# Optimization experiments

Measured on AMD Instinct MI355X. Metric: run time of the kernel, lower is better.

The kernel has to match this reference:

```python
import jax, jax.numpy as jnp
from jax import lax
import numpy as np

NPOINT, RADIUS, NSAMPLE = 1024, 0.2, 32
MLP = [64, 64, 128]
IN_CH = 35  # 3 coord channels + 32 point features
EPS = 1e-5


def farthest_point_sample(xyz, npoint):
    # xyz: (B, N, 3) -> (B, npoint) int32. Deterministic start at index 0.
    B, N, _ = xyz.shape

    def step(carry, _):
        dist, farthest = carry  # (B,N), (B,)
        centroid = jnp.take_along_axis(xyz, farthest[:, None, None], axis=1)  # (B,1,3)
        d = jnp.sum((xyz - centroid) ** 2, axis=-1)  # (B,N)
        dist = jnp.minimum(dist, d)
        nxt = jnp.argmax(dist, axis=-1).astype(jnp.int32)
        return (dist, nxt), farthest

    init = (jnp.full((B, N), 1e10, xyz.dtype), jnp.zeros((B,), jnp.int32))
    _, idxs = lax.scan(step, init, None, length=npoint)
    return idxs.T  # (B, npoint)


def gather_points(points, idx):
    # points: (B, N, C); idx: (B, ...) int -> (B, ..., C)
    return jax.vmap(lambda p, i: p[i])(points, idx)


def query_ball_point(radius, nsample, xyz, new_xyz):
    # xyz: (B,N,3), new_xyz: (B,S,3) -> (B,S,nsample) int32
    B, N, _ = xyz.shape
    sqrdists = jnp.sum((new_xyz[:, :, None, :] - xyz[:, None, :, :]) ** 2, axis=-1)  # (B,S,N)
    group_idx = jnp.where(sqrdists > radius ** 2, N, jnp.arange(N, dtype=jnp.int32))
    group_idx = jnp.sort(group_idx, axis=-1)[:, :, :nsample]
    first = group_idx[:, :, :1]
    return jnp.where(group_idx == N, first, group_idx)


def sa_forward(xyz, points, params):
    B, N, C = xyz.shape
    fps_idx = farthest_point_sample(xyz, NPOINT)
    new_xyz = gather_points(xyz, fps_idx)  # (B,S,3)
    idx = query_ball_point(RADIUS, NSAMPLE, xyz, new_xyz)  # (B,S,K)
    grouped_xyz = gather_points(xyz, idx)  # (B,S,K,3)
    grouped_xyz_norm = grouped_xyz - new_xyz[:, :, None, :]
    grouped_points = gather_points(points, idx)  # (B,S,K,D)
    new_points = jnp.concatenate([grouped_xyz_norm, grouped_points], axis=-1)  # (B,S,K,Cin)
    x = new_points.transpose(0, 3, 2, 1)  # (B, Cin, K, S)
    for w, b, g, be in params:
        x = jnp.einsum('oi,biks->boks', w, x) + b[None, :, None, None]  # 1x1 conv
        mean = x.mean(axis=(0, 2, 3), keepdims=True)  # BatchNorm2d, training mode
        var = x.var(axis=(0, 2, 3), keepdims=True)
        x = (x - mean) / jnp.sqrt(var + EPS)
        x = jax.nn.relu(g[None, :, None, None] * x + be[None, :, None, None])
    new_points_out = x.max(axis=2)  # max over nsample -> (B, Cout, S)
    return new_xyz, new_points_out


def setup_inputs() -> dict:
    key = jax.random.key(0)
    ks = jax.random.split(key, 16)
    B, N, D = 16, 4096, 32
    inp = {
        'xyz': jax.random.uniform(ks[0], (B, N, 3), dtype=jnp.float32),
        'points': jax.random.normal(ks[1], (B, N, D), dtype=jnp.float32),
    }
    last = IN_CH
    for li, out_ch in enumerate(MLP):
        inp[f'w{li}'] = jax.random.normal(ks[2 + 4 * li], (out_ch, last), dtype=jnp.float32) * 0.05
        inp[f'b{li}'] = jnp.zeros((out_ch,), jnp.float32)
        inp[f'g{li}'] = jnp.ones((out_ch,), jnp.float32)
        inp[f'be{li}'] = jnp.zeros((out_ch,), jnp.float32)
        last = out_ch
    return inp


def reference(xyz, points, w0, b0, g0, be0, w1, b1, g1, be1, w2, b2, g2, be2):
    params = [(w0, b0, g0, be0), (w1, b1, g1, be1), (w2, b2, g2, be2)]
    return sa_forward(xyz, points, params)
```

## Files before the change

### kernel.cpp

```cpp
#include <hip/hip_runtime.h>
#include <hip/hip_bf16.h>
#include <stdint.h>

#pragma clang fp contract(off)

#define BATCH   16
#define NPTS    4096
#define NPOINT  1024
#define NSAMPLE 32
#define NPOS    (BATCH*NPOINT*NSAMPLE)
#define NBLK    (NPOS/128)
#define NGRP    (BATCH*NPOINT)
#define EPSV    1e-5f

typedef unsigned short ushort_t;
typedef unsigned int uint_t;
typedef unsigned long long u64;
typedef __attribute__((ext_vector_type(8))) short bf16x8;
typedef __attribute__((ext_vector_type(4))) float f32x4;
typedef __attribute__((ext_vector_type(2))) float f32x2;

__device__ inline ushort_t f2bf(float f) {
    uint_t u = __float_as_uint(f);
    u += 0x7fffu + ((u >> 16) & 1u);
    return (ushort_t)(u >> 16);
}
__device__ inline uint_t pkbf(float a, float b) {
    __hip_bfloat162 h = __float22bfloat162_rn(make_float2(a, b));
    uint_t r; __builtin_memcpy(&r, &h, 4); return r;
}
__device__ inline bf16x8 asbf(uint4 u) {
    bf16x8 v; __builtin_memcpy(&v, &u, 16); return v;
}
__device__ inline void unpack8(uint4 u, float* f) {
    f[0] = __uint_as_float(u.x << 16); f[1] = __uint_as_float(u.x & 0xffff0000u);
    f[2] = __uint_as_float(u.y << 16); f[3] = __uint_as_float(u.y & 0xffff0000u);
    f[4] = __uint_as_float(u.z << 16); f[5] = __uint_as_float(u.z & 0xffff0000u);
    f[6] = __uint_as_float(u.w << 16); f[7] = __uint_as_float(u.w & 0xffff0000u);
}

__global__ __launch_bounds__(256) void prep_w(const float* __restrict__ w0,
                                              const float* __restrict__ w1,
                                              const float* __restrict__ w2,
                                              ushort_t* __restrict__ Wp0,
                                              ushort_t* __restrict__ Wx0,
                                              ushort_t* __restrict__ Wp1,
                                              ushort_t* __restrict__ Wp2) {
    const int t = blockIdx.x * 256 + threadIdx.x;
    const int stride = gridDim.x * 256;
    for (int i = t; i < 64 * 32; i += stride) { int ch = i >> 5, k = i & 31; Wp0[i] = f2bf(w0[ch * 35 + 3 + k]); }
    for (int i = t; i < 64 * 4;  i += stride) { int ch = i >> 2, q = i & 3;  Wx0[i] = (q < 3) ? f2bf(w0[ch * 35 + q]) : (ushort_t)0; }
    for (int i = t; i < 64 * 64; i += stride) Wp1[i] = f2bf(w1[i]);
    for (int i = t; i < 128 * 64; i += stride) Wp2[i] = f2bf(w2[i]);
}

#define DPP_MAX_STAGE(CTRL) do {                                              \
    uint_t _lo2 = __builtin_amdgcn_update_dpp(lo, lo, CTRL, 0xf, 0xf, false); \
    uint_t _hi2 = __builtin_amdgcn_update_dpp(hi, hi, CTRL, 0xf, 0xf, false); \
    u64 _o = ((u64)_hi2 << 32) | _lo2;                                        \
    u64 _v = ((u64)hi << 32) | lo;                                            \
    bool _g = _o > _v;                                                        \
    lo = _g ? _lo2 : lo; hi = _g ? _hi2 : hi;                                 \
} while (0)

__global__ __launch_bounds__(256) void fps_kernel(const float* __restrict__ xyz,
                                                  float* __restrict__ new_xyz) {
    __shared__ float4 lxyz[NPTS];
    __shared__ u64 wbest[2][4];
    __shared__ int fpsidx[NPOINT];
    const int b = blockIdx.x;
    const int tid = threadIdx.x;
    const float* base = xyz + (size_t)b * NPTS * 3;
    for (int n = tid; n < NPTS; n += 256) {
        lxyz[n] = make_float4(base[3 * n], base[3 * n + 1], base[3 * n + 2], 0.f);
    }
    __syncthreads();

    f32x2 px[8], py[8], pz[8], dist[8];
    uint_t lowc[16];
#pragma unroll
    for (int j = 0; j < 8; j++) {
        float4 v0 = lxyz[tid + (2 * j) * 256];
        float4 v1 = lxyz[tid + (2 * j + 1) * 256];
        px[j] = (f32x2){v0.x, v1.x};
        py[j] = (f32x2){v0.y, v1.y};
        pz[j] = (f32x2){v0.z, v1.z};
        dist[j] = (f32x2){1e10f, 1e10f};
        lowc[2 * j] = ~(uint_t)(tid + (2 * j) * 256);
        lowc[2 * j + 1] = ~(uint_t)(tid + (2 * j + 1) * 256);
    }
    if (tid == 0) fpsidx[0] = 0;
    int cur = 0;
    const int lane = tid & 63, wid = tid >> 6;

    for (int it = 1; it < NPOINT; ++it) {
        float4 c = lxyz[cur];
        const f32x2 cx = (f32x2){c.x, c.x};
        const f32x2 cy = (f32x2){c.y, c.y};
        const f32x2 cz = (f32x2){c.z, c.z};
        u64 t[8];
#pragma unroll
        for (int j = 0; j < 8; j++) {
            f32x2 dx = px[j] - cx;
            f32x2 dy = py[j] - cy;
            f32x2 dz = pz[j] - cz;
            f32x2 d = (dx * dx + dy * dy) + dz * dz;
            f32x2 nd = __builtin_elementwise_min(dist[j], d);
            dist[j] = nd;
            u64 e0 = ((u64)__float_as_uint(nd.x) << 32) | lowc[2 * j];
            u64 e1 = ((u64)__float_as_uint(nd.y) << 32) | lowc[2 * j + 1];
            t[j] = e0 > e1 ? e0 : e1;
        }
#pragma unroll
        for (int j = 0; j < 4; j++) { u64 o = t[j + 4]; t[j] = t[j] > o ? t[j] : o; }
        t[0] = t[0] > t[1] ? t[0] : t[1];
        t[2] = t[2] > t[3] ? t[2] : t[3];
        u64 v = t[0] > t[2] ? t[0] : t[2];

        uint_t lo = (uint_t)v, hi = (uint_t)(v >> 32);
        DPP_MAX_STAGE(0x111);
        DPP_MAX_STAGE(0x112);
        DPP_MAX_STAGE(0x114);
        DPP_MAX_STAGE(0x118);
        DPP_MAX_STAGE(0x142);
        DPP_MAX_STAGE(0x143);
        uint_t mlo = __builtin_amdgcn_readlane(lo, 63);
        uint_t mhi = __builtin_amdgcn_readlane(hi, 63);

        const int par = it & 1;
        if (lane == 0) wbest[par][wid] = ((u64)mhi << 32) | mlo;
        __syncthreads();
        u64 b0 = wbest[par][0], b1 = wbest[par][1];
        u64 b2 = wbest[par][2], b3 = wbest[par][3];
        u64 m01 = b0 > b1 ? b0 : b1;
        u64 m23 = b2 > b3 ? b2 : b3;
        u64 bb = m01 > m23 ? m01 : m23;
        cur = (int)(~(uint_t)bb) & (NPTS - 1);
        if (tid == 0) fpsidx[it] = cur;
    }
    __syncthreads();
    float* ob = new_xyz + (size_t)b * NPOINT * 3;
    for (int s = tid; s < NPOINT; s += 256) {
        float4 v = lxyz[fpsidx[s]];
        ob[3 * s + 0] = v.x; ob[3 * s + 1] = v.y; ob[3 * s + 2] = v.z;
    }
}

__global__ __launch_bounds__(256) void ballq_kernel(const float* __restrict__ xyz,
                                                    const float* __restrict__ new_xyz,
                                                    int* __restrict__ gidx) {
    const int gw = (int)((blockIdx.x * 256 + threadIdx.x) >> 6);
    const int lane = threadIdx.x & 63;
    const int b = gw / NPOINT, s = gw % NPOINT;
    const float* nb = new_xyz + ((size_t)b * NPOINT + s) * 3;
    const float cx = nb[0], cy = nb[1], cz = nb[2];
    const float* xb = xyz + (size_t)b * NPTS * 3;
    const float r2 = (float)(0.2 * 0.2);
    int cnt = 0;
    int first = -1;
    int* out = gidx + (size_t)gw * NSAMPLE;
    for (int j0 = 0; j0 < NPTS; j0 += 64) {
        int j = j0 + lane;
        float dx = __fsub_rn(xb[j * 3 + 0], cx);
        float dy = __fsub_rn(xb[j * 3 + 1], cy);
        float dz = __fsub_rn(xb[j * 3 + 2], cz);
        float d = __fadd_rn(__fadd_rn(__fmul_rn(dx, dx), __fmul_rn(dy, dy)),
                            __fmul_rn(dz, dz));
        bool pred = !(d > r2);
        u64 mask = __ballot(pred);
        if (first < 0 && mask != 0ull) first = j0 + (__ffsll((long long)mask) - 1);
        int before = __popcll(mask & ((1ull << lane) - 1ull));
        int slot = cnt + before;
        if (pred && slot < NSAMPLE) out[slot] = j;
        cnt += (int)__popcll(mask);
        if (cnt >= NSAMPLE) break;
    }
    if (cnt < NSAMPLE) {
        if (lane >= cnt && lane < NSAMPLE) out[lane] = first;
    }
}

__global__ __launch_bounds__(256) void conv1_mfma(const float* __restrict__ xyz,
                                                  const float* __restrict__ points,
                                                  const float* __restrict__ new_xyz,
                                                  const int* __restrict__ gidx,
                                                  const ushort_t* __restrict__ Wp0,
                                                  const ushort_t* __restrict__ Wx0,
                                                  const float* __restrict__ bias,
                                                  ushort_t* __restrict__ Y,
                                                  float* __restrict__ part_s,
                                                  float* __restrict__ part_q) {
    const int lane = threadIdx.x & 63, wid = threadIdx.x >> 6;
    const int l15 = lane & 15, quad = lane >> 4;
    const int p0 = blockIdx.x * 128 + wid * 32;

    bf16x8 Bp[4], Bx[4];
#pragma unroll
    for (int nt = 0; nt < 4; nt++) {
        const int ch = nt * 16 + l15;
        Bp[nt] = *(const bf16x8*)(Wp0 + (size_t)ch * 32 + quad * 8);
        uint4 bx = {0u, 0u, 0u, 0u};
        if (quad == 0) {
            uint2 wv = *(const uint2*)(Wx0 + ch * 4);
            bx.x = wv.x; bx.y = wv.y;
        }
        Bx[nt] = asbf(bx);
    }
    f32x4 acc[2][4];
#pragma unroll
    for (int mt = 0; mt < 2; mt++)
#pragma unroll
        for (int nt = 0; nt < 4; nt++) acc[mt][nt] = (f32x4){0.f, 0.f, 0.f, 0.f};

#pragma unroll
    for (int mt = 0; mt < 2; mt++) {
        const int p = p0 + mt * 16 + l15;
        const int b = p >> 15, s = (p & 32767) >> 5;
        const int j = gidx[p];
        const float* pr = points + ((size_t)(b * NPTS + j)) * 32 + quad * 8;
        float4 pa = *(const float4*)pr;
        float4 pb4 = *(const float4*)(pr + 4);
        uint4 ap;
        ap.x = pkbf(pa.x, pa.y);  ap.y = pkbf(pa.z, pa.w);
        ap.z = pkbf(pb4.x, pb4.y); ap.w = pkbf(pb4.z, pb4.w);
        bf16x8 Ap = asbf(ap);
        uint4 ax = {0u, 0u, 0u, 0u};
        if (quad == 0) {
            const float* xp = xyz + ((size_t)(b * NPTS + j)) * 3;
            const float* nz = new_xyz + ((size_t)(b * NPOINT + s)) * 3;
            float d0 = xp[0] - nz[0], d1 = xp[1] - nz[1], d2 = xp[2] - nz[2];
            ax.x = pkbf(d0, d1);
            ax.y = pkbf(d2, 0.f);
        }
        bf16x8 Ax = asbf(ax);
#pragma unroll
        for (int nt = 0; nt < 4; nt++) {
            acc[mt][nt] = __builtin_amdgcn_mfma_f32_16x16x32_bf16(Ap, Bp[nt], acc[mt][nt], 0, 0, 0);
            acc[mt][nt] = __builtin_amdgcn_mfma_f32_16x16x32_bf16(Ax, Bx[nt], acc[mt][nt], 0, 0, 0);
        }
    }
    float s_[4], q_[4];
#pragma unroll
    for (int nt = 0; nt < 4; nt++) { s_[nt] = 0.f; q_[nt] = 0.f; }
#pragma unroll
    for (int nt = 0; nt < 4; nt++) {
        const int ch = nt * 16 + l15;
        const float bs = bias[ch];
#pragma unroll
        for (int mt = 0; mt < 2; mt++) {
            const int pb = p0 + mt * 16 + quad * 4;
            float x0 = acc[mt][nt][0] + bs, x1 = acc[mt][nt][1] + bs;
            float x2 = acc[mt][nt][2] + bs, x3 = acc[mt][nt][3] + bs;
            uint_t p01 = pkbf(x0, x1), p23 = pkbf(x2, x3);
            Y[(size_t)(pb + 0) * 64 + ch] = (ushort_t)(p01 & 0xffffu);
            Y[(size_t)(pb + 1) * 64 + ch] = (ushort_t)(p01 >> 16);
            Y[(size_t)(pb + 2) * 64 + ch] = (ushort_t)(p23 & 0xffffu);
            Y[(size_t)(pb + 3) * 64 + ch] = (ushort_t)(p23 >> 16);
            float v0 = __uint_as_float(p01 << 16), v1 = __uint_as_float(p01 & 0xffff0000u);
            float v2 = __uint_as_float(p23 << 16), v3 = __uint_as_float(p23 & 0xffff0000u);
            s_[nt] += (v0 + v1) + (v2 + v3);
            q_[nt] += (v0 * v0 + v1 * v1) + (v2 * v2 + v3 * v3);
        }
    }
#pragma unroll
    for (int nt = 0; nt < 4; nt++) {
        s_[nt] += __shfl_xor(s_[nt], 16, 64); s_[nt] += __shfl_xor(s_[nt], 32, 64);
        q_[nt] += __shfl_xor(q_[nt], 16, 64); q_[nt] += __shfl_xor(q_[nt], 32, 64);
    }
    __shared__ float reds[4][4][16], redq[4][4][16];
    if (lane < 16) {
#pragma unroll
        for (int nt = 0; nt < 4; nt++) { reds[wid][nt][lane] = s_[nt]; redq[wid][nt][lane] = q_[nt]; }
    }
    __syncthreads();
    if (threadIdx.x < 16) {
#pragma unroll
        for (int nt = 0; nt < 4; nt++) {
            float ss = 0.f, qq = 0.f;
#pragma unroll
            for (int w = 0; w < 4; w++) { ss += reds[w][nt][threadIdx.x]; qq += redq[w][nt][threadIdx.x]; }
            const int ch = nt * 16 + threadIdx.x;
            part_s[(size_t)ch * NBLK + blockIdx.x] = ss;
            part_q[(size_t)ch * NBLK + blockIdx.x] = qq;
        }
    }
}

__global__ __launch_bounds__(256) void conv2_mfma(const ushort_t* __restrict__ Yin,
                                                  const float* __restrict__ scale,
                                                  const float* __restrict__ shift,
                                                  const ushort_t* __restrict__ Wp,
                                                  const float* __restrict__ bias,
                                                  ushort_t* __restrict__ Yout,
                                                  float* __restrict__ part_s,
                                                  float* __restrict__ part_q) {
    constexpr int IN = 64, OUT = 64, NT = 4;
    const int lane = threadIdx.x & 63, wid = threadIdx.x >> 6;
    const int l15 = lane & 15, quad = lane >> 4;
    const int p0 = blockIdx.x * 128 + wid * 32;

    float sc[2][8], sh[2][8];
#pragma unroll
    for (int kq = 0; kq < 2; kq++) {
        const int i0 = kq * 32 + quad * 8;
#pragma unroll
        for (int q = 0; q < 8; q++) { sc[kq][q] = scale[i0 + q]; sh[kq][q] = shift[i0 + q]; }
    }
    bf16x8 Bf[NT][2];
#pragma unroll
    for (int nt = 0; nt < NT; nt++)
#pragma unroll
        for (int kq = 0; kq < 2; kq++)
            Bf[nt][kq] = *(const bf16x8*)(Wp + (size_t)(nt * 16 + l15) * IN + kq * 32 + quad * 8);

    bf16x8 Af[2][2];
#pragma unroll
    for (int mt = 0; mt < 2; mt++)
#pragma unroll
        for (int kq = 0; kq < 2; kq++) {
            const ushort_t* yr = Yin + (size_t)(p0 + mt * 16 + l15) * IN + kq * 32 + quad * 8;
            uint4 u = *(const uint4*)yr;
            float f[8]; unpack8(u, f);
            float g0 = fmaxf(fmaf(f[0], sc[kq][0], sh[kq][0]), 0.f);
            float g1 = fmaxf(fmaf(f[1], sc[kq][1], sh[kq][1]), 0.f);
            float g2 = fmaxf(fmaf(f[2], sc[kq][2], sh[kq][2]), 0.f);
            float g3 = fmaxf(fmaf(f[3], sc[kq][3], sh[kq][3]), 0.f);
            float g4 = fmaxf(fmaf(f[4], sc[kq][4], sh[kq][4]), 0.f);
            float g5 = fmaxf(fmaf(f[5], sc[kq][5], sh[kq][5]), 0.f);
            float g6 = fmaxf(fmaf(f[6], sc[kq][6], sh[kq][6]), 0.f);
            float g7 = fmaxf(fmaf(f[7], sc[kq][7], sh[kq][7]), 0.f);
            uint4 a;
            a.x = pkbf(g0, g1); a.y = pkbf(g2, g3);
            a.z = pkbf(g4, g5); a.w = pkbf(g6, g7);
            Af[mt][kq] = asbf(a);
        }

    f32x4 acc[2][NT];
#pragma unroll
    for (int mt = 0; mt < 2; mt++)
#pragma unroll
        for (int nt = 0; nt < NT; nt++) acc[mt][nt] = (f32x4){0.f, 0.f, 0.f, 0.f};
#pragma unroll
    for (int mt = 0; mt < 2; mt++)
#pragma unroll
        for (int nt = 0; nt < NT; nt++) {
            acc[mt][nt] = __builtin_amdgcn_mfma_f32_16x16x32_bf16(Af[mt][0], Bf[nt][0], acc[mt][nt], 0, 0, 0);
            acc[mt][nt] = __builtin_amdgcn_mfma_f32_16x16x32_bf16(Af[mt][1], Bf[nt][1], acc[mt][nt], 0, 0, 0);
        }
    float s_[NT], q_[NT];
#pragma unroll
    for (int nt = 0; nt < NT; nt++) { s_[nt] = 0.f; q_[nt] = 0.f; }
#pragma unroll
    for (int nt = 0; nt < NT; nt++) {
        const int ch = nt * 16 + l15;
        const float bs = bias[ch];
#pragma unroll
        for (int mt = 0; mt < 2; mt++) {
            const int pb = p0 + mt * 16 + quad * 4;
            float x0 = acc[mt][nt][0] + bs, x1 = acc[mt][nt][1] + bs;
            float x2 = acc[mt][nt][2] + bs, x3 = acc[mt][nt][3] + bs;
            uint_t p01 = pkbf(x0, x1), p23 = pkbf(x2, x3);
            Yout[(size_t)(pb + 0) * OUT + ch] = (ushort_t)(p01 & 0xffffu);
            Yout[(size_t)(pb + 1) * OUT + ch] = (ushort_t)(p01 >> 16);
            Yout[(size_t)(pb + 2) * OUT + ch] = (ushort_t)(p23 & 0xffffu);
            Yout[(size_t)(pb + 3) * OUT + ch] = (ushort_t)(p23 >> 16);
            float v0 = __uint_as_float(p01 << 16), v1 = __uint_as_float(p01 & 0xffff0000u);
            float v2 = __uint_as_float(p23 << 16), v3 = __uint_as_float(p23 & 0xffff0000u);
            s_[nt] += (v0 + v1) + (v2 + v3);
            q_[nt] += (v0 * v0 + v1 * v1) + (v2 * v2 + v3 * v3);
        }
    }
#pragma unroll
    for (int nt = 0; nt < NT; nt++) {
        s_[nt] += __shfl_xor(s_[nt], 16, 64); s_[nt] += __shfl_xor(s_[nt], 32, 64);
        q_[nt] += __shfl_xor(q_[nt], 16, 64); q_[nt] += __shfl_xor(q_[nt], 32, 64);
    }
    __shared__ float reds[4][NT][16], redq[4][NT][16];
    if (lane < 16) {
#pragma unroll
        for (int nt = 0; nt < NT; nt++) { reds[wid][nt][lane] = s_[nt]; redq[wid][nt][lane] = q_[nt]; }
    }
    __syncthreads();
    if (threadIdx.x < 16) {
#pragma unroll
        for (int nt = 0; nt < NT; nt++) {
            float ss = 0.f, qq = 0.f;
#pragma unroll
            for (int w = 0; w < 4; w++) { ss += reds[w][nt][threadIdx.x]; qq += redq[w][nt][threadIdx.x]; }
            const int ch = nt * 16 + threadIdx.x;
            part_s[(size_t)ch * NBLK + blockIdx.x] = ss;
            part_q[(size_t)ch * NBLK + blockIdx.x] = qq;
        }
    }
}

__global__ __launch_bounds__(256) void conv3_mfma(const ushort_t* __restrict__ Yin,
                                                  const float* __restrict__ scale,
                                                  const float* __restrict__ shift,
                                                  const ushort_t* __restrict__ Wp,
                                                  const float* __restrict__ bias,
                                                  float* __restrict__ xmax,
                                                  float* __restrict__ xmin,
                                                  float* __restrict__ part_s,
                                                  float* __restrict__ part_q) {
    constexpr int IN = 64, NT = 8;
    const int lane = threadIdx.x & 63, wid = threadIdx.x >> 6;
    const int l15 = lane & 15, quad = lane >> 4;
    const int p0 = blockIdx.x * 128 + wid * 32;
    const int g = p0 >> 5;

    float sc[2][8], sh[2][8];
#pragma unroll
    for (int kq = 0; kq < 2; kq++) {
        const int i0 = kq * 32 + quad * 8;
#pragma unroll
        for (int q = 0; q < 8; q++) { sc[kq][q] = scale[i0 + q]; sh[kq][q] = shift[i0 + q]; }
    }
    bf16x8 Bf[NT][2];
#pragma unroll
    for (int nt = 0; nt < NT; nt++)
#pragma unroll
        for (int kq = 0; kq < 2; kq++)
            Bf[nt][kq] = *(const bf16x8*)(Wp + (size_t)(nt * 16 + l15) * IN + kq * 32 + quad * 8);

    bf16x8 Af[2][2];
#pragma unroll
    for (int mt = 0; mt < 2; mt++)
#pragma unroll
        for (int kq = 0; kq < 2; kq++) {
            const ushort_t* yr = Yin + (size_t)(p0 + mt * 16 + l15) * IN + kq * 32 + quad * 8;
            uint4 u = *(const uint4*)yr;
            float f[8]; unpack8(u, f);
            float g0 = fmaxf(fmaf(f[0], sc[kq][0], sh[kq][0]), 0.f);
            float g1 = fmaxf(fmaf(f[1], sc[kq][1], sh[kq][1]), 0.f);
            float g2 = fmaxf(fmaf(f[2], sc[kq][2], sh[kq][2]), 0.f);
            float g3 = fmaxf(fmaf(f[3], sc[kq][3], sh[kq][3]), 0.f);
            float g4 = fmaxf(fmaf(f[4], sc[kq][4], sh[kq][4]), 0.f);
            float g5 = fmaxf(fmaf(f[5], sc[kq][5], sh[kq][5]), 0.f);
            float g6 = fmaxf(fmaf(f[6], sc[kq][6], sh[kq][6]), 0.f);
            float g7 = fmaxf(fmaf(f[7], sc[kq][7], sh[kq][7]), 0.f);
            uint4 a;
            a.x = pkbf(g0, g1); a.y = pkbf(g2, g3);
            a.z = pkbf(g4, g5); a.w = pkbf(g6, g7);
            Af[mt][kq] = asbf(a);
        }

    f32x4 acc[2][NT];
#pragma unroll
    for (int mt = 0; mt < 2; mt++)
#pragma unroll
        for (int nt = 0; nt < NT; nt++) acc[mt][nt] = (f32x4){0.f, 0.f, 0.f, 0.f};
#pragma unroll
    for (int mt = 0; mt < 2; mt++)
#pragma unroll
        for (int nt = 0; nt < NT; nt++) {
            acc[mt][nt] = __builtin_amdgcn_mfma_f32_16x16x32_bf16(Af[mt][0], Bf[nt][0], acc[mt][nt], 0, 0, 0);
            acc[mt][nt] = __builtin_amdgcn_mfma_f32_16x16x32_bf16(Af[mt][1], Bf[nt][1], acc[mt][nt], 0, 0, 0);
        }
    float s_[NT], q_[NT], xm[NT], xn[NT];
#pragma unroll
    for (int nt = 0; nt < NT; nt++) { s_[nt] = 0.f; q_[nt] = 0.f; xm[nt] = -3e38f; xn[nt] = 3e38f; }
#pragma unroll
    for (int nt = 0; nt < NT; nt++) {
        const float bs = bias[nt * 16 + l15];
#pragma unroll
        for (int mt = 0; mt < 2; mt++) {
#pragma unroll
            for (int r = 0; r < 4; r++) {
                float x = acc[mt][nt][r] + bs;
                s_[nt] += x; q_[nt] += x * x;
                xm[nt] = fmaxf(xm[nt], x); xn[nt] = fminf(xn[nt], x);
            }
        }
    }
#pragma unroll
    for (int nt = 0; nt < NT; nt++) {
        s_[nt] += __shfl_xor(s_[nt], 16, 64); s_[nt] += __shfl_xor(s_[nt], 32, 64);
        q_[nt] += __shfl_xor(q_[nt], 16, 64); q_[nt] += __shfl_xor(q_[nt], 32, 64);
        xm[nt] = fmaxf(xm[nt], __shfl_xor(xm[nt], 16, 64));
        xm[nt] = fmaxf(xm[nt], __shfl_xor(xm[nt], 32, 64));
        xn[nt] = fminf(xn[nt], __shfl_xor(xn[nt], 16, 64));
        xn[nt] = fminf(xn[nt], __shfl_xor(xn[nt], 32, 64));
    }
    if (quad == 0) {
#pragma unroll
        for (int nt = 0; nt < NT; nt++) {
            const int ch = nt * 16 + l15;
            xmax[(size_t)g * 128 + ch] = xm[nt];
            xmin[(size_t)g * 128 + ch] = xn[nt];
        }
    }
    __shared__ float reds[4][NT][16], redq[4][NT][16];
    if (lane < 16) {
#pragma unroll
        for (int nt = 0; nt < NT; nt++) { reds[wid][nt][lane] = s_[nt]; redq[wid][nt][lane] = q_[nt]; }
    }
    __syncthreads();
    if (threadIdx.x < 16) {
#pragma unroll
        for (int nt = 0; nt < NT; nt++) {
            float ss = 0.f, qq = 0.f;
#pragma unroll
            for (int w = 0; w < 4; w++) { ss += reds[w][nt][threadIdx.x]; qq += redq[w][nt][threadIdx.x]; }
            const int ch = nt * 16 + threadIdx.x;
            part_s[(size_t)ch * NBLK + blockIdx.x] = ss;
            part_q[(size_t)ch * NBLK + blockIdx.x] = qq;
        }
    }
}

__global__ __launch_bounds__(256) void reduce_finalize(const float* __restrict__ part_s,
                                                       const float* __restrict__ part_q,
                                                       const float* __restrict__ g,
                                                       const float* __restrict__ be,
                                                       float* __restrict__ scale,
                                                       float* __restrict__ shift) {
    const int ch = blockIdx.x;
    const float* p1 = part_s + (size_t)ch * NBLK;
    const float* p2 = part_q + (size_t)ch * NBLK;
    float s = 0.f, q = 0.f;
    for (int i = threadIdx.x; i < NBLK; i += 256) { s += p1[i]; q += p2[i]; }
#pragma unroll
    for (int m = 1; m < 64; m <<= 1) { s += __shfl_xor(s, m, 64); q += __shfl_xor(q, m, 64); }
    __shared__ float ls[4], lq[4];
    const int lane = threadIdx.x & 63, wid = threadIdx.x >> 6;
    if (lane == 0) { ls[wid] = s; lq[wid] = q; }
    __syncthreads();
    if (threadIdx.x == 0) {
        float ssum = ls[0] + ls[1] + ls[2] + ls[3];
        float qsum = lq[0] + lq[1] + lq[2] + lq[3];
        float mean = ssum * (1.f / (float)NPOS);
        float var = qsum * (1.f / (float)NPOS) - mean * mean;
        float inv = 1.f / sqrtf(var + EPSV);
        float sc = g[ch] * inv;
        scale[ch] = sc;
        shift[ch] = be[ch] - mean * sc;
    }
}

__global__ __launch_bounds__(256) void final2_kernel(const float* __restrict__ xmax,
                                                     const float* __restrict__ xmin,
                                                     const float* __restrict__ scale,
                                                     const float* __restrict__ shift,
                                                     float* __restrict__ out) {
    __shared__ float buf[128][129];
    const int b = blockIdx.x >> 3;
    const int s0 = (blockIdx.x & 7) * 128;
    const int tid = threadIdx.x;
    for (int i = tid; i < 128 * 128; i += 256) {
        const int si = i >> 7, ch = i & 127;
        const size_t g = (size_t)(b * NPOINT + s0 + si);
        const float sc = scale[ch], sh = shift[ch];
        const float xM = xmax[g * 128 + ch];
        const float xN = xmin[g * 128 + ch];
        const float X = sc > 0.f ? xM : xN;
        buf[si][ch] = fmaxf(fmaf(X, sc, sh), 0.f);
    }
    __syncthreads();
    for (int i = tid; i < 128 * 128; i += 256) {
        const int ch = i >> 7, si = i & 127;
        out[((size_t)(b * 128 + ch)) * NPOINT + s0 + si] = buf[si][ch];
    }
}

extern "C" void kernel_launch(void* const* d_in, const int* in_sizes, int n_in,
                              void* d_out, int out_size, void* d_ws, size_t ws_size,
                              hipStream_t stream) {
    const float* xyz = (const float*)d_in[0];
    const float* points = (const float*)d_in[1];
    const float* w0 = (const float*)d_in[2];
    const float* b0 = (const float*)d_in[3];
    const float* g0 = (const float*)d_in[4];
    const float* be0 = (const float*)d_in[5];
    const float* w1 = (const float*)d_in[6];
    const float* b1 = (const float*)d_in[7];
    const float* g1 = (const float*)d_in[8];
    const float* be1 = (const float*)d_in[9];
    const float* w2 = (const float*)d_in[10];
    const float* b2 = (const float*)d_in[11];
    const float* g2 = (const float*)d_in[12];
    const float* be2 = (const float*)d_in[13];

    float* out = (float*)d_out;
    float* new_xyz = out;
    float* final_out = out + BATCH * NPOINT * 3;

    char* ws = (char*)d_ws;
    const size_t MB = 1024u * 1024u;
    const size_t o_gidx = 0;
    const size_t o_y2 = 2 * MB;
    const size_t o_y1 = o_y2 + (size_t)NPOS * 64 * 2;
    const size_t o_params = o_y1 + (size_t)NPOS * 64 * 2;
    const size_t o_parts = o_params + 4096;
    const size_t o_w = o_parts + 4 * MB;
    const size_t o_xm = o_w + 64 * 1024;
    const size_t o_xn = o_xm + (size_t)NGRP * 128 * 4;

    int* gidx = (int*)(ws + o_gidx);
    ushort_t* Y1 = (ushort_t*)(ws + o_y1);
    ushort_t* Y2 = (ushort_t*)(ws + o_y2);
    float* pr = (float*)(ws + o_params);
    float* scale1 = pr + 0, *shift1 = pr + 64;
    float* scale2 = pr + 128, *shift2 = pr + 192;
    float* scale3 = pr + 256, *shift3 = pr + 384;
    float* part_s = (float*)(ws + o_parts);
    float* part_q = part_s + (size_t)128 * NBLK;
    ushort_t* Wp0 = (ushort_t*)(ws + o_w);
    ushort_t* Wx0 = Wp0 + 64 * 32;
    ushort_t* Wp1 = Wx0 + 64 * 4;
    ushort_t* Wp2 = Wp1 + 64 * 64;
    float* xmax = (float*)(ws + o_xm);
    float* xmin = (float*)(ws + o_xn);

    prep_w<<<8, 256, 0, stream>>>(w0, w1, w2, Wp0, Wx0, Wp1, Wp2);
    fps_kernel<<<BATCH, 256, 0, stream>>>(xyz, new_xyz);
    ballq_kernel<<<(BATCH * NPOINT) / 4, 256, 0, stream>>>(xyz, new_xyz, gidx);
    conv1_mfma<<<NBLK, 256, 0, stream>>>(xyz, points, new_xyz, gidx, Wp0, Wx0, b0, Y1, part_s, part_q);
    reduce_finalize<<<64, 256, 0, stream>>>(part_s, part_q, g0, be0, scale1, shift1);
    conv2_mfma<<<NBLK, 256, 0, stream>>>(Y1, scale1, shift1, Wp1, b1, Y2, part_s, part_q);
    reduce_finalize<<<64, 256, 0, stream>>>(part_s, part_q, g1, be1, scale2, shift2);
    conv3_mfma<<<NBLK, 256, 0, stream>>>(Y2, scale2, shift2, Wp2, b2, xmax, xmin, part_s, part_q);
    reduce_finalize<<<128, 256, 0, stream>>>(part_s, part_q, g2, be2, scale3, shift3);
    final2_kernel<<<128, 256, 0, stream>>>(xmax, xmin, scale3, shift3, final_out);
}
```

Measured before the change: 890.9 us.

## Replace FPS per-iteration barrier with tagged LDS spin-wait and fold weight prep

The farthest-point-sampling loop previously used a __syncthreads per iteration to exchange the four per-wave maxima. It now tags each wave's packed key with the iteration number in bits 12 and up of the low word, storing the index as 4095-idx in the low 12 bits, and every wave spin-polls the volatile LDS slots until all four carry the current tag. This removes the full block barrier from the serial 1023-step critical path. Weight bf16 conversion is also folded into an extra block of the FPS launch, removing one kernel launch. The spin-wait relies on LDS ordering and on the two-slot parity buffer being safe against a fast wave overwriting a slot still being read, and the tag bits only fit while the iteration count stays below 2^20.

```diff
diff --git a/kernel.cpp b/kernel.cpp
--- a/kernel.cpp
+++ b/kernel.cpp
@@ -39,21 +39,6 @@
     f[6] = __uint_as_float(u.w << 16); f[7] = __uint_as_float(u.w & 0xffff0000u);
 }
 
-__global__ __launch_bounds__(256) void prep_w(const float* __restrict__ w0,
-                                              const float* __restrict__ w1,
-                                              const float* __restrict__ w2,
-                                              ushort_t* __restrict__ Wp0,
-                                              ushort_t* __restrict__ Wx0,
-                                              ushort_t* __restrict__ Wp1,
-                                              ushort_t* __restrict__ Wp2) {
-    const int t = blockIdx.x * 256 + threadIdx.x;
-    const int stride = gridDim.x * 256;
-    for (int i = t; i < 64 * 32; i += stride) { int ch = i >> 5, k = i & 31; Wp0[i] = f2bf(w0[ch * 35 + 3 + k]); }
-    for (int i = t; i < 64 * 4;  i += stride) { int ch = i >> 2, q = i & 3;  Wx0[i] = (q < 3) ? f2bf(w0[ch * 35 + q]) : (ushort_t)0; }
-    for (int i = t; i < 64 * 64; i += stride) Wp1[i] = f2bf(w1[i]);
-    for (int i = t; i < 128 * 64; i += stride) Wp2[i] = f2bf(w2[i]);
-}
-
 #define DPP_MAX_STAGE(CTRL) do {                                              \
     uint_t _lo2 = __builtin_amdgcn_update_dpp(lo, lo, CTRL, 0xf, 0xf, false); \
     uint_t _hi2 = __builtin_amdgcn_update_dpp(hi, hi, CTRL, 0xf, 0xf, false); \
@@ -64,7 +49,22 @@
 } while (0)
 
 __global__ __launch_bounds__(256) void fps_kernel(const float* __restrict__ xyz,
-                                                  float* __restrict__ new_xyz) {
+                                                  float* __restrict__ new_xyz,
+                                                  const float* __restrict__ w0,
+                                                  const float* __restrict__ w1,
+                                                  const float* __restrict__ w2,
+                                                  ushort_t* __restrict__ Wp0,
+                                                  ushort_t* __restrict__ Wx0,
+                                                  ushort_t* __restrict__ Wp1,
+                                                  ushort_t* __restrict__ Wp2) {
+    if (blockIdx.x == 16) {
+        const int t = threadIdx.x;
+        for (int i = t; i < 64 * 32; i += 256) { int ch = i >> 5, k = i & 31; Wp0[i] = f2bf(w0[ch * 35 + 3 + k]); }
+        for (int i = t; i < 64 * 4;  i += 256) { int ch = i >> 2, q = i & 3;  Wx0[i] = (q < 3) ? f2bf(w0[ch * 35 + q]) : (ushort_t)0; }
+        for (int i = t; i < 64 * 64; i += 256) Wp1[i] = f2bf(w1[i]);
+        for (int i = t; i < 128 * 64; i += 256) Wp2[i] = f2bf(w2[i]);
+        return;
+    }
     __shared__ float4 lxyz[NPTS];
     __shared__ u64 wbest[2][4];
     __shared__ int fpsidx[NPOINT];
@@ -74,6 +74,7 @@
     for (int n = tid; n < NPTS; n += 256) {
         lxyz[n] = make_float4(base[3 * n], base[3 * n + 1], base[3 * n + 2], 0.f);
     }
+    if (tid < 8) ((u64*)wbest)[tid] = 0;
     __syncthreads();
 
     f32x2 px[8], py[8], pz[8], dist[8];
@@ -86,8 +87,8 @@
         py[j] = (f32x2){v0.y, v1.y};
         pz[j] = (f32x2){v0.z, v1.z};
         dist[j] = (f32x2){1e10f, 1e10f};
-        lowc[2 * j] = ~(uint_t)(tid + (2 * j) * 256);
-        lowc[2 * j + 1] = ~(uint_t)(tid + (2 * j + 1) * 256);
+        lowc[2 * j] = (uint_t)(4095 - (tid + (2 * j) * 256));
+        lowc[2 * j + 1] = (uint_t)(4095 - (tid + (2 * j + 1) * 256));
     }
     if (tid == 0) fpsidx[0] = 0;
     int cur = 0;
@@ -128,14 +129,20 @@
         uint_t mhi = __builtin_amdgcn_readlane(hi, 63);
 
         const int par = it & 1;
-        if (lane == 0) wbest[par][wid] = ((u64)mhi << 32) | mlo;
-        __syncthreads();
-        u64 b0 = wbest[par][0], b1 = wbest[par][1];
-        u64 b2 = wbest[par][2], b3 = wbest[par][3];
+        volatile u64* wb = &wbest[par][0];
+        if (lane == 0)
+            wb[wid] = (((u64)mhi << 32) | mlo) + ((u64)it << 12);
+        u64 b0, b1, b2, b3;
+        do {
+            b0 = wb[0]; b1 = wb[1]; b2 = wb[2]; b3 = wb[3];
+        } while ((((uint_t)b0 >> 12) != (uint_t)it) |
+                 (((uint_t)b1 >> 12) != (uint_t)it) |
+                 (((uint_t)b2 >> 12) != (uint_t)it) |
+                 (((uint_t)b3 >> 12) != (uint_t)it));
         u64 m01 = b0 > b1 ? b0 : b1;
         u64 m23 = b2 > b3 ? b2 : b3;
         u64 bb = m01 > m23 ? m01 : m23;
-        cur = (int)(~(uint_t)bb) & (NPTS - 1);
+        cur = 4095 - (int)((uint_t)bb & 0xFFFu);
         if (tid == 0) fpsidx[it] = cur;
     }
     __syncthreads();
@@ -612,8 +619,7 @@
     float* xmax = (float*)(ws + o_xm);
     float* xmin = (float*)(ws + o_xn);
 
-    prep_w<<<8, 256, 0, stream>>>(w0, w1, w2, Wp0, Wx0, Wp1, Wp2);
-    fps_kernel<<<BATCH, 256, 0, stream>>>(xyz, new_xyz);
+    fps_kernel<<<17, 256, 0, stream>>>(xyz, new_xyz, w0, w1, w2, Wp0, Wx0, Wp1, Wp2);
     ballq_kernel<<<(BATCH * NPOINT) / 4, 256, 0, stream>>>(xyz, new_xyz, gidx);
     conv1_mfma<<<NBLK, 256, 0, stream>>>(xyz, points, new_xyz, gidx, Wp0, Wx0, b0, Y1, part_s, part_q);
     reduce_finalize<<<64, 256, 0, stream>>>(part_s, part_q, g0, be0, scale1, shift1);
```

Result: slower. 1.013 ms (+13.7%).

## Pack two FPS batches per block and fold weight prep into FPS launch

Applied to the files above, without the earlier changes.

The farthest-point-sampling kernel now runs two batch elements per 512-thread block, each half using its own shared-memory slice, and an extra ninth block converts the weights to bf16, which removes the separate prep_w launch. The __syncthreads inside the iteration loop now synchronises both halves together, coupling two independent serial chains. FPS is a latency-bound serial loop, so the barrier across 8 waves may lengthen each iteration. The main saving is one kernel launch.

```diff
diff --git a/kernel.cpp b/kernel.cpp
--- a/kernel.cpp
+++ b/kernel.cpp
@@ -39,21 +39,6 @@
     f[6] = __uint_as_float(u.w << 16); f[7] = __uint_as_float(u.w & 0xffff0000u);
 }
 
-__global__ __launch_bounds__(256) void prep_w(const float* __restrict__ w0,
-                                              const float* __restrict__ w1,
-                                              const float* __restrict__ w2,
-                                              ushort_t* __restrict__ Wp0,
-                                              ushort_t* __restrict__ Wx0,
-                                              ushort_t* __restrict__ Wp1,
-                                              ushort_t* __restrict__ Wp2) {
-    const int t = blockIdx.x * 256 + threadIdx.x;
-    const int stride = gridDim.x * 256;
-    for (int i = t; i < 64 * 32; i += stride) { int ch = i >> 5, k = i & 31; Wp0[i] = f2bf(w0[ch * 35 + 3 + k]); }
-    for (int i = t; i < 64 * 4;  i += stride) { int ch = i >> 2, q = i & 3;  Wx0[i] = (q < 3) ? f2bf(w0[ch * 35 + q]) : (ushort_t)0; }
-    for (int i = t; i < 64 * 64; i += stride) Wp1[i] = f2bf(w1[i]);
-    for (int i = t; i < 128 * 64; i += stride) Wp2[i] = f2bf(w2[i]);
-}
-
 #define DPP_MAX_STAGE(CTRL) do {                                              \
     uint_t _lo2 = __builtin_amdgcn_update_dpp(lo, lo, CTRL, 0xf, 0xf, false); \
     uint_t _hi2 = __builtin_amdgcn_update_dpp(hi, hi, CTRL, 0xf, 0xf, false); \
@@ -63,16 +48,32 @@
     lo = _g ? _lo2 : lo; hi = _g ? _hi2 : hi;                                 \
 } while (0)
 
-__global__ __launch_bounds__(256) void fps_kernel(const float* __restrict__ xyz,
-                                                  float* __restrict__ new_xyz) {
-    __shared__ float4 lxyz[NPTS];
-    __shared__ u64 wbest[2][4];
-    __shared__ int fpsidx[NPOINT];
-    const int b = blockIdx.x;
-    const int tid = threadIdx.x;
+__global__ __launch_bounds__(512) void fps_kernel(const float* __restrict__ xyz,
+                                                  float* __restrict__ new_xyz,
+                                                  const float* __restrict__ w0,
+                                                  const float* __restrict__ w1,
+                                                  const float* __restrict__ w2,
+                                                  ushort_t* __restrict__ Wp0,
+                                                  ushort_t* __restrict__ Wx0,
+                                                  ushort_t* __restrict__ Wp1,
+                                                  ushort_t* __restrict__ Wp2) {
+    if (blockIdx.x == 8) {
+        const int t = threadIdx.x;
+        for (int i = t; i < 64 * 32; i += 512) { int ch = i >> 5, k = i & 31; Wp0[i] = f2bf(w0[ch * 35 + 3 + k]); }
+        for (int i = t; i < 64 * 4;  i += 512) { int ch = i >> 2, q = i & 3;  Wx0[i] = (q < 3) ? f2bf(w0[ch * 35 + q]) : (ushort_t)0; }
+        for (int i = t; i < 64 * 64; i += 512) Wp1[i] = f2bf(w1[i]);
+        for (int i = t; i < 128 * 64; i += 512) Wp2[i] = f2bf(w2[i]);
+        return;
+    }
+    __shared__ float4 lxyz[2][NPTS];
+    __shared__ u64 wbest[2][2][4];
+    __shared__ int fpsidx[2][NPOINT];
+    const int g = threadIdx.x >> 8;
+    const int tid = threadIdx.x & 255;
+    const int b = blockIdx.x * 2 + g;
     const float* base = xyz + (size_t)b * NPTS * 3;
     for (int n = tid; n < NPTS; n += 256) {
-        lxyz[n] = make_float4(base[3 * n], base[3 * n + 1], base[3 * n + 2], 0.f);
+        lxyz[g][n] = make_float4(base[3 * n], base[3 * n + 1], base[3 * n + 2], 0.f);
     }
     __syncthreads();
 
@@ -80,8 +81,8 @@
     uint_t lowc[16];
 #pragma unroll
     for (int j = 0; j < 8; j++) {
-        float4 v0 = lxyz[tid + (2 * j) * 256];
-        float4 v1 = lxyz[tid + (2 * j + 1) * 256];
+        float4 v0 = lxyz[g][tid + (2 * j) * 256];
+        float4 v1 = lxyz[g][tid + (2 * j + 1) * 256];
         px[j] = (f32x2){v0.x, v1.x};
         py[j] = (f32x2){v0.y, v1.y};
         pz[j] = (f32x2){v0.z, v1.z};
@@ -89,12 +90,12 @@
         lowc[2 * j] = ~(uint_t)(tid + (2 * j) * 256);
         lowc[2 * j + 1] = ~(uint_t)(tid + (2 * j + 1) * 256);
     }
-    if (tid == 0) fpsidx[0] = 0;
+    if (tid == 0) fpsidx[g][0] = 0;
     int cur = 0;
     const int lane = tid & 63, wid = tid >> 6;
 
     for (int it = 1; it < NPOINT; ++it) {
-        float4 c = lxyz[cur];
+        float4 c = lxyz[g][cur];
         const f32x2 cx = (f32x2){c.x, c.x};
         const f32x2 cy = (f32x2){c.y, c.y};
         const f32x2 cz = (f32x2){c.z, c.z};
@@ -128,20 +129,20 @@
         uint_t mhi = __builtin_amdgcn_readlane(hi, 63);
 
         const int par = it & 1;
-        if (lane == 0) wbest[par][wid] = ((u64)mhi << 32) | mlo;
+        if (lane == 0) wbest[g][par][wid] = ((u64)mhi << 32) | mlo;
         __syncthreads();
-        u64 b0 = wbest[par][0], b1 = wbest[par][1];
-        u64 b2 = wbest[par][2], b3 = wbest[par][3];
+        u64 b0 = wbest[g][par][0], b1 = wbest[g][par][1];
+        u64 b2 = wbest[g][par][2], b3 = wbest[g][par][3];
         u64 m01 = b0 > b1 ? b0 : b1;
         u64 m23 = b2 > b3 ? b2 : b3;
         u64 bb = m01 > m23 ? m01 : m23;
         cur = (int)(~(uint_t)bb) & (NPTS - 1);
-        if (tid == 0) fpsidx[it] = cur;
+        if (tid == 0) fpsidx[g][it] = cur;
     }
     __syncthreads();
     float* ob = new_xyz + (size_t)b * NPOINT * 3;
     for (int s = tid; s < NPOINT; s += 256) {
-        float4 v = lxyz[fpsidx[s]];
+        float4 v = lxyz[g][fpsidx[g][s]];
         ob[3 * s + 0] = v.x; ob[3 * s + 1] = v.y; ob[3 * s + 2] = v.z;
     }
 }
@@ -612,8 +613,7 @@
     float* xmax = (float*)(ws + o_xm);
     float* xmin = (float*)(ws + o_xn);
 
-    prep_w<<<8, 256, 0, stream>>>(w0, w1, w2, Wp0, Wx0, Wp1, Wp2);
-    fps_kernel<<<BATCH, 256, 0, stream>>>(xyz, new_xyz);
+    fps_kernel<<<9, 512, 0, stream>>>(xyz, new_xyz, w0, w1, w2, Wp0, Wx0, Wp1, Wp2);
     ballq_kernel<<<(BATCH * NPOINT) / 4, 256, 0, stream>>>(xyz, new_xyz, gidx);
     conv1_mfma<<<NBLK, 256, 0, stream>>>(xyz, points, new_xyz, gidx, Wp0, Wx0, b0, Y1, part_s, part_q);
     reduce_finalize<<<64, 256, 0, stream>>>(part_s, part_q, g0, be0, scale1, shift1);
```

Result: slower. 1.163 ms (+30.6%).
